# Kernel optimization log

Hardware: AMD Instinct MI355X
Metric: run time of the kernel (lower is better)

## Reference

```python
import jax, jax.numpy as jnp
import numpy as np

NUM_CLASSES = 4
LAMBDA_CREDA = 1.0
LAMBDA_ENTROPY = 0.1
SIGMA = 32.0          # config.sigma (fixed, not 'auto')
USE_UNCERTAINTY = True
EPS = 1e-8
LOG2 = float(np.log(2.0))

N_S, N_T, D = 4096, 4096, 1024


def _rbf(x, y, sigma):
    # squared euclidean distances (== torch.cdist(x,y)**2), then gaussian kernel
    d2 = (jnp.sum(x * x, axis=1)[:, None] + jnp.sum(y * y, axis=1)[None, :]
          - 2.0 * (x @ y.T))
    d2 = jnp.maximum(d2, 0.0)
    return jnp.exp(-d2 / (2.0 * sigma * sigma + EPS))


def _h2(tr, sumsq):
    # H2(A) = -log2(tr(A@A)), A = K/(tr(K)+eps); tr(A@A) = sum(K*K)/(tr+eps)^2 for symmetric K
    info = sumsq / (tr + EPS) ** 2
    return -jnp.log(info + EPS) / LOG2


def setup_inputs() -> dict:
    key = jax.random.key(0)
    k1, k2, k3, k4, k5 = jax.random.split(key, 5)
    return {
        "features_s": jax.random.normal(k1, (N_S, D), dtype=jnp.float32),
        "logits_s": jax.random.normal(k2, (N_S, NUM_CLASSES), dtype=jnp.float32),
        "features_t": jax.random.normal(k3, (N_T, D), dtype=jnp.float32),
        "logits_t": jax.random.normal(k4, (N_T, NUM_CLASSES), dtype=jnp.float32),
        "labels_s": jax.random.randint(k5, (N_S,), 0, NUM_CLASSES, dtype=jnp.int32),
    }


def reference(features_s, logits_s, features_t, logits_t, labels_s):
    # ---- classification loss (cross entropy on source) ----
    logp_s = jax.nn.log_softmax(logits_s, axis=1)
    loss_cls = -jnp.mean(jnp.take_along_axis(logp_s, labels_s[:, None], axis=1))

    # ---- target entropy loss ----
    probs_t = jax.nn.softmax(logits_t, axis=1)
    loss_ent = -jnp.mean(jnp.sum(probs_t * jnp.log(probs_t + EPS), axis=1))

    # ---- pseudo labels + uncertainty weights ----
    pseudo_t = jnp.argmax(jax.lax.stop_gradient(probs_t), axis=1)
    if USE_UNCERTAINTY:
        h2_probs = -jnp.log(jnp.sum(probs_t ** 2, axis=1) + EPS) / LOG2
        h2_max = np.log(float(NUM_CLASSES)) / LOG2
        w = 1.0 - h2_probs / (h2_max + EPS)          # [N_t]
    else:
        w = jnp.ones((features_t.shape[0],), dtype=probs_t.dtype)

    # ---- shared RBF kernel blocks (sigma fixed -> identical across classes) ----
    K_ss = _rbf(features_s, features_s, SIGMA)       # [N_s, N_s]
    K_tt = _rbf(features_t, features_t, SIGMA)       # [N_t, N_t]
    K_st = _rbf(features_s, features_t, SIGMA)       # [N_s, N_t]

    # per-class masks (zero-masking a kernel preserves trace and trace(K@K))
    Ms = jax.nn.one_hot(labels_s, NUM_CLASSES, dtype=K_ss.dtype).T   # [C, N_s]
    Mt = jax.nn.one_hot(pseudo_t, NUM_CLASSES, dtype=K_tt.dtype).T   # [C, N_t]
    Wt = Mt * w[None, :]                                             # [C, N_t]
    Wt2 = Wt * Wt

    n_s = jnp.sum(Ms, axis=1)                        # class counts (source)
    n_t = jnp.sum(Mt, axis=1)                        # class counts (target)

    # traces: diag(K)=1, target block weighted by outer(w,w)
    tr_s = n_s                                       # [C]
    tr_t = jnp.sum(Wt2, axis=1)                      # [C]

    # sum of squared entries of the masked (and weighted) blocks
    ss_s = jnp.einsum('ci,ci->c', Ms @ (K_ss ** 2), Ms)     # tr(K_s^2) per class
    ss_t = jnp.einsum('ci,ci->c', Wt2 @ (K_tt ** 2), Wt2)   # tr(K_tw^2) per class
    ss_st = jnp.einsum('ci,ci->c', Ms @ (K_st ** 2), Mt)    # sum(K_st^2) per class

    h_s = _h2(tr_s, ss_s)
    h_t = _h2(tr_t, ss_t)
    h_mix = _h2(tr_s + tr_t, ss_s + 2.0 * ss_st + ss_t)

    per_class = h_mix - 0.5 * (h_s + h_t)            # [C]
    valid = (n_s >= 2) & (n_t >= 2)
    n_valid = jnp.sum(valid.astype(per_class.dtype))
    creda_sum = jnp.sum(jnp.where(valid, per_class, 0.0))
    loss_creda = jnp.where(n_valid > 0, creda_sum / jnp.maximum(n_valid, 1.0), 0.0)

    total_loss = loss_cls + LAMBDA_CREDA * loss_creda + LAMBDA_ENTROPY * loss_ent
    return total_loss
```

## Files before the change

kernel.cpp:

```cpp
#include <hip/hip_runtime.h>
#include <cstdint>
#include <cstddef>

#define NS_ROWS 4096
#define NT_ROWS 4096
#define DIM 1024
#define NC 4
#define NWORK_MAX 2432
#define ACC_N 26

typedef __attribute__((ext_vector_type(4))) float f32x4;
typedef long long i64;

#define GLOBAL_AS __attribute__((address_space(1)))
#define LDS_AS __attribute__((address_space(3)))


__device__ __forceinline__ int argmax4(float4 l) {
    int am = 0; float bm = l.x;
    if (l.y > bm) { bm = l.y; am = 1; }
    if (l.z > bm) { bm = l.z; am = 2; }
    if (l.w > bm) { bm = l.w; am = 3; }
    return am;
}

__global__ void prep_rows(const float* __restrict__ LS, const int* __restrict__ labels,
                          const float* __restrict__ LT, float* __restrict__ acc) {
    __shared__ float sacc[ACC_N];
    int t = threadIdx.x;
    if (t < ACC_N) sacc[t] = 0.f;
    __syncthreads();
    int gid = blockIdx.x * 256 + t;
    const float EPSF = 1e-8f;
    if (gid < NS_ROWS) {
        float4 l = ((const float4*)LS)[gid];
        float m = fmaxf(fmaxf(l.x, l.y), fmaxf(l.z, l.w));
        float e = expf(l.x - m) + expf(l.y - m) + expf(l.z - m) + expf(l.w - m);
        float lse = m + logf(e);
        int lab = labels[gid];
        float ll = (lab == 0) ? l.x : (lab == 1) ? l.y : (lab == 2) ? l.z : l.w;
        atomicAdd(&sacc[0], lse - ll);
    } else {
        int j = gid - NS_ROWS;
        float4 l = ((const float4*)LT)[j];
        float m = fmaxf(fmaxf(l.x, l.y), fmaxf(l.z, l.w));
        float p0 = expf(l.x - m), p1 = expf(l.y - m), p2 = expf(l.z - m), p3 = expf(l.w - m);
        float s = p0 + p1 + p2 + p3;
        p0 /= s; p1 /= s; p2 /= s; p3 /= s;
        float ent = p0 * logf(p0 + EPSF) + p1 * logf(p1 + EPSF) +
                    p2 * logf(p2 + EPSF) + p3 * logf(p3 + EPSF);
        int am = argmax4(l);
        float sumsq = p0 * p0 + p1 * p1 + p2 * p2 + p3 * p3;
        const float INV_LOG2 = 1.44269504088896340736f;
        float h2 = -logf(sumsq + EPSF) * INV_LOG2;
        float w = 1.0f - h2 / (2.0f + EPSF);
        atomicAdd(&sacc[1], ent);
        atomicAdd(&sacc[10 + am], w * w);
    }
    __syncthreads();
    if (t < ACC_N && sacc[t] != 0.f) atomicAdd(&acc[t], sacc[t]);
}

__global__ void rank_rows(const int* __restrict__ labels, const float* __restrict__ LT,
                          int* __restrict__ ctrl, float* __restrict__ acc,
                          int* __restrict__ dstS, int* __restrict__ dstT) {
    __shared__ unsigned long long sdata[1024];
    int t = threadIdx.x;
    bool isS = (blockIdx.x == 0);
    int* dst = isS ? dstS : dstT;

    int c4[4];
    if (isS) {
        int4 lab4 = ((const int4*)labels)[t];
        c4[0] = lab4.x; c4[1] = lab4.y; c4[2] = lab4.z; c4[3] = lab4.w;
        if (t < ACC_N) acc[t] = 0.f;
    } else {
#pragma unroll
        for (int i = 0; i < 4; ++i)
            c4[i] = argmax4(((const float4*)LT)[t * 4 + i]);
    }
    unsigned long long packed = 0ULL;
#pragma unroll
    for (int i = 0; i < 4; ++i) packed += 1ULL << (c4[i] * 16);
    sdata[t] = packed;
    __syncthreads();
    for (int off = 1; off < 1024; off <<= 1) {
        unsigned long long v = sdata[t];
        unsigned long long add = (t >= off) ? sdata[t - off] : 0ULL;
        __syncthreads();
        sdata[t] = v + add;
        __syncthreads();
    }
    unsigned long long tot = sdata[1023];
    unsigned long long ex = (t > 0) ? sdata[t - 1] : 0ULL;
    int baseC[NC]; int b = 0;
#pragma unroll
    for (int c = 0; c < NC; ++c) {
        baseC[c] = b;
        b += (int)((tot >> (c * 16)) & 0xFFFFULL);
    }
    if (t == 0) {
#pragma unroll
        for (int c = 0; c < NC; ++c) {
            ctrl[(isS ? 0 : 4) + c] = (int)((tot >> (c * 16)) & 0xFFFFULL);
            ctrl[(isS ? 16 : 20) + c] = baseC[c];
        }
    }
    int pref[NC];
#pragma unroll
    for (int c = 0; c < NC; ++c)
        pref[c] = (int)((ex >> (c * 16)) & 0xFFFFULL) + baseC[c];
#pragma unroll
    for (int i = 0; i < 4; ++i) {
        int c = c4[i];
        dst[t * 4 + i] = pref[c]++;
    }
}

__global__ void aux_build(const int* __restrict__ ctrl, int4* __restrict__ wl,
                          int* __restrict__ ctrl_w) {
    int t = threadIdx.x;
    int Ts[NC], Tt[NC];
#pragma unroll
    for (int c = 0; c < NC; ++c) {
        Ts[c] = (ctrl[c] + 127) >> 7;
        Tt[c] = (ctrl[4 + c] + 127) >> 7;
    }
    int segSize[12];
#pragma unroll
    for (int c = 0; c < NC; ++c) {
        segSize[c * 3 + 0] = Ts[c] * (Ts[c] + 1) / 2;
        segSize[c * 3 + 1] = Tt[c] * (Tt[c] + 1) / 2;
        segSize[c * 3 + 2] = Ts[c] * Tt[c];
    }
    if (t == 0) {
        int n = 0;
        for (int s = 0; s < 12; ++s) n += segSize[s];
        ctrl_w[24] = n;
    }
    if (t >= 12) return;
    int base = 0;
    for (int s = 0; s < t; ++s) base += segSize[s];
    int c = t / 3, kind = t % 3;
    int4* w = wl + base;
    int n = 0;
    if (kind == 0) {
        for (int tj = 0; tj < Ts[c]; ++tj)
            for (int ti = 0; ti <= tj; ++ti) w[n++] = make_int4(0, c, ti, tj);
    } else if (kind == 1) {
        for (int tj = 0; tj < Tt[c]; ++tj)
            for (int ti = 0; ti <= tj; ++ti) w[n++] = make_int4(1, c, ti, tj);
    } else {
        for (int ti = 0; ti < Ts[c]; ++ti)
            for (int tj = 0; tj < Tt[c]; ++tj) w[n++] = make_int4(2, c, ti, tj);
    }
}

__global__ void scatter_feat(const float* __restrict__ FS, const float* __restrict__ FT,
                             const int* __restrict__ labels, const float* __restrict__ LT,
                             const int* __restrict__ dstS, const int* __restrict__ dstT,
                             unsigned char* __restrict__ fs, unsigned char* __restrict__ ft,
                             float* __restrict__ nS, float* __restrict__ wS, int* __restrict__ cS,
                             float* __restrict__ nT, float* __restrict__ wT, int* __restrict__ cT) {
    int row = blockIdx.x * 4 + (threadIdx.x >> 6);
    int lane = threadIdx.x & 63;
    bool isS = row < NS_ROWS;
    int r = isS ? row : row - NS_ROWS;
    int dst = isS ? dstS[r] : dstT[r];

    const float* src = (isS ? FS : FT) + (size_t)r * DIM;
    float4 v0 = ((const float4*)src)[lane * 4 + 0];
    float4 v1 = ((const float4*)src)[lane * 4 + 1];
    float4 v2 = ((const float4*)src)[lane * 4 + 2];
    float4 v3 = ((const float4*)src)[lane * 4 + 3];
    int w0 = 0, w1 = 0, w2 = 0, w3 = 0;
    w0 = __builtin_amdgcn_cvt_pk_fp8_f32(v0.x, v0.y, w0, false);
    w0 = __builtin_amdgcn_cvt_pk_fp8_f32(v0.z, v0.w, w0, true);
    w1 = __builtin_amdgcn_cvt_pk_fp8_f32(v1.x, v1.y, w1, false);
    w1 = __builtin_amdgcn_cvt_pk_fp8_f32(v1.z, v1.w, w1, true);
    w2 = __builtin_amdgcn_cvt_pk_fp8_f32(v2.x, v2.y, w2, false);
    w2 = __builtin_amdgcn_cvt_pk_fp8_f32(v2.z, v2.w, w2, true);
    w3 = __builtin_amdgcn_cvt_pk_fp8_f32(v3.x, v3.y, w3, false);
    w3 = __builtin_amdgcn_cvt_pk_fp8_f32(v3.z, v3.w, w3, true);

    float ssum = 0.f;
#define ACCQ(wv)                                                       \
    do {                                                               \
        float q0 = __builtin_amdgcn_cvt_f32_fp8((wv), 0);              \
        float q1 = __builtin_amdgcn_cvt_f32_fp8((wv), 1);              \
        float q2 = __builtin_amdgcn_cvt_f32_fp8((wv), 2);              \
        float q3 = __builtin_amdgcn_cvt_f32_fp8((wv), 3);              \
        ssum += q0 * q0 + q1 * q1 + q2 * q2 + q3 * q3;                 \
    } while (0)
    ACCQ(w0); ACCQ(w1); ACCQ(w2); ACCQ(w3);
#undef ACCQ

    unsigned char* fdst = (isS ? fs : ft) + (size_t)dst * DIM;
    *(uint4*)(fdst + lane * 16) = make_uint4((unsigned)w0, (unsigned)w1,
                                             (unsigned)w2, (unsigned)w3);

    for (int off = 32; off; off >>= 1) ssum += __shfl_xor(ssum, off);

    if (lane == 0) {
        if (isS) {
            nS[dst] = ssum; wS[dst] = 1.0f; cS[dst] = labels[r];
        } else {
            float4 l = ((const float4*)LT)[r];
            int am = argmax4(l);
            float m = fmaxf(fmaxf(l.x, l.y), fmaxf(l.z, l.w));
            float p0 = expf(l.x - m), p1 = expf(l.y - m),
                  p2 = expf(l.z - m), p3 = expf(l.w - m);
            float s = p0 + p1 + p2 + p3;
            float sumsq = (p0 * p0 + p1 * p1 + p2 * p2 + p3 * p3) / (s * s);
            const float INV_LOG2 = 1.44269504088896340736f;
            float h2 = -logf(sumsq + 1e-8f) * INV_LOG2;
            float w = 1.0f - h2 / (2.0f + 1e-8f);
            nT[dst] = ssum; wT[dst] = w * w; cT[dst] = am;
        }
    }
}

__global__ __launch_bounds__(256, 4)
void gemm_reduce(const unsigned char* __restrict__ fs, const unsigned char* __restrict__ ft,
                 const float* __restrict__ nS, const float* __restrict__ wS, const int* __restrict__ cS,
                 const float* __restrict__ nT, const float* __restrict__ wT, const int* __restrict__ cT,
                 const int* __restrict__ ctrl, const int4* __restrict__ wl,
                 float* __restrict__ acc) {
    __shared__ unsigned char As[2][128 * 32];
    __shared__ unsigned char Bs[2][128 * 32];
    __shared__ float sred;

    int nwork = ctrl[24];
    int chunk = (nwork + 7) >> 3;
    int sub = blockIdx.x >> 3, xcd = blockIdx.x & 7;
    if (sub >= chunk) return;
    int widx = xcd * chunk + sub;
    if (widx >= nwork) return;
    int4 it = wl[widx];
    int kind = it.x, cls = it.y, ti = it.z, tj = it.w;

    const unsigned char *A, *B;
    const float *nA, *nB, *wA, *wB;
    const int *cA, *cB;
    int baseA, baseB;
    if (kind == 0)      { A = fs; B = fs; nA = nS; nB = nS; wA = wS; wB = wS; cA = cS; cB = cS;
                          baseA = ctrl[16 + cls]; baseB = baseA; }
    else if (kind == 1) { A = ft; B = ft; nA = nT; nB = nT; wA = wT; wB = wT; cA = cT; cB = cT;
                          baseA = ctrl[20 + cls]; baseB = baseA; }
    else                { A = fs; B = ft; nA = nS; nB = nT; wA = wS; cA = cS; cB = cT;
                          wB = wS;
                          baseA = ctrl[16 + cls]; baseB = ctrl[20 + cls]; }
    float* outp = acc + 14 + kind * 4 + cls;
    float factor = (kind != 2 && ti != tj) ? 2.0f : 1.0f;

    int tid = threadIdx.x;
    int lane = tid & 63;
    int wid = tid >> 6;
    int wr = wid >> 1, wc = wid & 1;

    int rowA0 = baseA + ti * 128;
    int rowB0 = baseB + tj * 128;

    int srow = tid >> 1;
    int sb = (tid & 1) * 16;

    const unsigned char* pa = A + (size_t)min(rowA0 + srow, 4095) * DIM + sb;
    const unsigned char* pb = B + (size_t)min(rowB0 + srow, 4095) * DIM + sb;

    f32x4 accf[4][4];
#pragma unroll
    for (int m = 0; m < 4; ++m)
#pragma unroll
        for (int n = 0; n < 4; ++n) accf[m][n] = (f32x4)(0.f);

    int lr = lane & 15;
    int lk = (lane >> 4) * 8;

#define STAGE(buf, kt)                                                            \
    do {                                                                          \
        int k0_ = (kt) * 32;                                                      \
        __builtin_amdgcn_global_load_lds((const GLOBAL_AS void*)(pa + k0_),       \
            (LDS_AS void*)(As[buf] + tid * 16), 16, 0, 0);                        \
        __builtin_amdgcn_global_load_lds((const GLOBAL_AS void*)(pb + k0_),       \
            (LDS_AS void*)(Bs[buf] + tid * 16), 16, 0, 0);                        \
    } while (0)

#define COMPUTE(buf)                                                              \
    do {                                                                          \
        i64 af[4], bfr[4];                                                        \
        _Pragma("unroll")                                                         \
        for (int f = 0; f < 4; ++f)                                               \
            af[f] = *(const i64*)(As[buf] + (wr * 64 + f * 16 + lr) * 32 + lk);   \
        _Pragma("unroll")                                                         \
        for (int f = 0; f < 4; ++f)                                               \
            bfr[f] = *(const i64*)(Bs[buf] + (wc * 64 + f * 16 + lr) * 32 + lk);  \
        _Pragma("unroll")                                                         \
        for (int m = 0; m < 4; ++m)                                               \
            _Pragma("unroll")                                                     \
            for (int n = 0; n < 4; ++n)                                           \
                accf[m][n] = __builtin_amdgcn_mfma_f32_16x16x32_fp8_fp8(          \
                    af[m], bfr[n], accf[m][n], 0, 0, 0);                          \
    } while (0)

    STAGE(0, 0);
    asm volatile("s_waitcnt vmcnt(0)");
    __syncthreads();

    int cur = 0;
    for (int kt = 0; kt < DIM / 32 - 1; ++kt) {
        STAGE(cur ^ 1, kt + 1);
        COMPUTE(cur);
        __syncthreads();
        cur ^= 1;
    }
    COMPUTE(cur);

    int rowBase = rowA0 + wr * 64;
    int colBase = rowB0 + wc * 64;

    float cn[4], cw[4];
#pragma unroll
    for (int f = 0; f < 4; ++f) {
        int gj = colBase + f * 16 + lr;
        int gjc = min(gj, 4095);
        cn[f] = nB[gjc];
        cw[f] = (gj < 4096 && cB[gjc] == cls) ? wB[gjc] : 0.0f;
    }

    const float NEGF = (-2.0f / (2.0f * 32.0f * 32.0f + 1e-8f)) * 1.44269504088896340736f;
    float lacc = 0.f;

#pragma unroll
    for (int m = 0; m < 4; ++m) {
#pragma unroll
        for (int j = 0; j < 4; ++j) {
            int gi = rowBase + m * 16 + (lane >> 4) * 4 + j;
            int gic = min(gi, 4095);
            float rn = nA[gic];
            float rw = (gi < 4096 && cA[gic] == cls) ? wA[gic] : 0.0f;
#pragma unroll
            for (int n = 0; n < 4; ++n) {
                float dot = accf[m][n][j];
                float d2 = rn + cn[n] - 2.0f * dot;
                d2 = fmaxf(d2, 0.0f);
                float k2 = exp2f(d2 * NEGF);
                lacc += k2 * rw * cw[n];
            }
        }
    }

    if (tid == 0) sred = 0.f;
    __syncthreads();
    for (int off = 32; off; off >>= 1) lacc += __shfl_xor(lacc, off);
    if (lane == 0) atomicAdd(&sred, lacc);
    __syncthreads();
    if (tid == 0) atomicAdd(outp, factor * sred);
#undef STAGE
#undef COMPUTE
}

__global__ void finalize_kernel(const float* __restrict__ acc, const int* __restrict__ ctrl,
                                float* __restrict__ out) {
    if (threadIdx.x != 0 || blockIdx.x != 0) return;
    const double EPS = 1e-8;
    const double LOG2 = 0.6931471805599453;
    double loss_cls = (double)acc[0] / NS_ROWS;
    double loss_ent = -(double)acc[1] / NT_ROWS;
    double creda_sum = 0.0, n_valid = 0.0;
    for (int c = 0; c < NC; ++c) {
        int nsc_i = ctrl[c], ntc_i = ctrl[4 + c];
        double nsc = (double)nsc_i, trt = acc[10 + c];
        double sss = acc[14 + c], sst = acc[18 + c], ssst = acc[22 + c];
        double trs = nsc;
        double info_s = sss / ((trs + EPS) * (trs + EPS));
        double h_s = -log(info_s + EPS) / LOG2;
        double info_t = sst / ((trt + EPS) * (trt + EPS));
        double h_t = -log(info_t + EPS) / LOG2;
        double trm = trs + trt;
        double ssm = sss + 2.0 * ssst + sst;
        double info_m = ssm / ((trm + EPS) * (trm + EPS));
        double h_m = -log(info_m + EPS) / LOG2;
        double pc = h_m - 0.5 * (h_s + h_t);
        if (nsc_i >= 2 && ntc_i >= 2) { creda_sum += pc; n_valid += 1.0; }
    }
    double creda = (n_valid > 0.0) ? creda_sum / n_valid : 0.0;
    out[0] = (float)(loss_cls + 1.0 * creda + 0.1 * loss_ent);
}

extern "C" void kernel_launch(void* const* d_in, const int* in_sizes, int n_in,
                              void* d_out, int out_size, void* d_ws, size_t ws_size,
                              hipStream_t stream) {
    const float* FS = (const float*)d_in[0];
    const float* LS = (const float*)d_in[1];
    const float* FT = (const float*)d_in[2];
    const float* LT = (const float*)d_in[3];
    const int* LAB = (const int*)d_in[4];

    char* ws = (char*)d_ws;
    unsigned char* fs = (unsigned char*)(ws);
    unsigned char* ft = (unsigned char*)(ws + 4194304);
    char* p = ws + 8388608;
    float* nS  = (float*)(p);
    float* wS  = (float*)(p + 16384);
    int*   cS  = (int*)  (p + 32768);
    float* nT  = (float*)(p + 49152);
    float* wT  = (float*)(p + 65536);
    int*   cT  = (int*)  (p + 81920);
    int*   ctrl = (int*)  (p + 98304);
    float* acc  = (float*)(p + 98304 + 128);
    int4*  wl   = (int4*) (p + 98304 + 512);
    int*   dstS = (int*)  (p + 98304 + 512 + NWORK_MAX * 16);
    int*   dstT = dstS + NS_ROWS;

    rank_rows<<<2, 1024, 0, stream>>>(LAB, LT, ctrl, acc, dstS, dstT);
    aux_build<<<1, 64, 0, stream>>>(ctrl, wl, ctrl);
    prep_rows<<<32, 256, 0, stream>>>(LS, LAB, LT, acc);
    scatter_feat<<<2048, 256, 0, stream>>>(FS, FT, LAB, LT, dstS, dstT, fs, ft,
                                           nS, wS, cS, nT, wT, cT);
    gemm_reduce<<<NWORK_MAX, 256, 0, stream>>>(fs, ft, nS, wS, cS, nT, wT, cT,
                                               ctrl, wl, acc);
    finalize_kernel<<<1, 1, 0, stream>>>(acc, ctrl, (float*)d_out);
}
```

Before: 70.24 us.

## Fuse row prep into rank kernel, use wave-shuffle scan, deepen GEMM K tile

Merges the separate prep_rows kernel into the ranking kernel, which removes one launch and its global atomics. The LDS Hillis-Steele scan with many barriers is replaced by a wave-level shuffle scan plus a small cross-wave scan. Zeroing of the accumulator slots moves into aux_build. The fp8 GEMM stages 64-wide K tiles instead of 32, halving the number of barriers and loop iterations, at the cost of twice the LDS per block, which may reduce occupancy.

```diff
diff --git a/kernel.cpp b/kernel.cpp
--- a/kernel.cpp
+++ b/kernel.cpp
@@ -24,75 +24,84 @@
     return am;
 }
 
-__global__ void prep_rows(const float* __restrict__ LS, const int* __restrict__ labels,
-                          const float* __restrict__ LT, float* __restrict__ acc) {
-    __shared__ float sacc[ACC_N];
+__global__ __launch_bounds__(1024)
+void rank_prep(const int* __restrict__ labels, const float* __restrict__ LS,
+               const float* __restrict__ LT,
+               int* __restrict__ ctrl, float* __restrict__ acc,
+               int* __restrict__ dstS, int* __restrict__ dstT) {
+    __shared__ unsigned long long wtot[16];
+    __shared__ float wred[16];
+    __shared__ float cls4[NC];
     int t = threadIdx.x;
-    if (t < ACC_N) sacc[t] = 0.f;
-    __syncthreads();
-    int gid = blockIdx.x * 256 + t;
-    const float EPSF = 1e-8f;
-    if (gid < NS_ROWS) {
-        float4 l = ((const float4*)LS)[gid];
-        float m = fmaxf(fmaxf(l.x, l.y), fmaxf(l.z, l.w));
-        float e = expf(l.x - m) + expf(l.y - m) + expf(l.z - m) + expf(l.w - m);
-        float lse = m + logf(e);
-        int lab = labels[gid];
-        float ll = (lab == 0) ? l.x : (lab == 1) ? l.y : (lab == 2) ? l.z : l.w;
-        atomicAdd(&sacc[0], lse - ll);
-    } else {
-        int j = gid - NS_ROWS;
-        float4 l = ((const float4*)LT)[j];
-        float m = fmaxf(fmaxf(l.x, l.y), fmaxf(l.z, l.w));
-        float p0 = expf(l.x - m), p1 = expf(l.y - m), p2 = expf(l.z - m), p3 = expf(l.w - m);
-        float s = p0 + p1 + p2 + p3;
-        p0 /= s; p1 /= s; p2 /= s; p3 /= s;
-        float ent = p0 * logf(p0 + EPSF) + p1 * logf(p1 + EPSF) +
-                    p2 * logf(p2 + EPSF) + p3 * logf(p3 + EPSF);
-        int am = argmax4(l);
-        float sumsq = p0 * p0 + p1 * p1 + p2 * p2 + p3 * p3;
-        const float INV_LOG2 = 1.44269504088896340736f;
-        float h2 = -logf(sumsq + EPSF) * INV_LOG2;
-        float w = 1.0f - h2 / (2.0f + EPSF);
-        atomicAdd(&sacc[1], ent);
-        atomicAdd(&sacc[10 + am], w * w);
-    }
-    __syncthreads();
-    if (t < ACC_N && sacc[t] != 0.f) atomicAdd(&acc[t], sacc[t]);
-}
-
-__global__ void rank_rows(const int* __restrict__ labels, const float* __restrict__ LT,
-                          int* __restrict__ ctrl, float* __restrict__ acc,
-                          int* __restrict__ dstS, int* __restrict__ dstT) {
-    __shared__ unsigned long long sdata[1024];
-    int t = threadIdx.x;
+    int wid = t >> 6, lane = t & 63;
     bool isS = (blockIdx.x == 0);
     int* dst = isS ? dstS : dstT;
+    const float EPSF = 1e-8f;
+    const float INV_LOG2 = 1.44269504088896340736f;
+
+    if (t < NC) cls4[t] = 0.f;
 
     int c4[4];
+    float localScalar = 0.f;
+    float localW2[NC] = {0.f, 0.f, 0.f, 0.f};
     if (isS) {
         int4 lab4 = ((const int4*)labels)[t];
         c4[0] = lab4.x; c4[1] = lab4.y; c4[2] = lab4.z; c4[3] = lab4.w;
-        if (t < ACC_N) acc[t] = 0.f;
+#pragma unroll
+        for (int i = 0; i < 4; ++i) {
+            float4 l = ((const float4*)LS)[t * 4 + i];
+            float m = fmaxf(fmaxf(l.x, l.y), fmaxf(l.z, l.w));
+            float e = expf(l.x - m) + expf(l.y - m) + expf(l.z - m) + expf(l.w - m);
+            float lse = m + logf(e);
+            int lab = c4[i];
+            float ll = (lab == 0) ? l.x : (lab == 1) ? l.y : (lab == 2) ? l.z : l.w;
+            localScalar += lse - ll;
+        }
     } else {
 #pragma unroll
-        for (int i = 0; i < 4; ++i)
-            c4[i] = argmax4(((const float4*)LT)[t * 4 + i]);
-    }
+        for (int i = 0; i < 4; ++i) {
+            float4 l = ((const float4*)LT)[t * 4 + i];
+            int am = argmax4(l);
+            c4[i] = am;
+            float m = fmaxf(fmaxf(l.x, l.y), fmaxf(l.z, l.w));
+            float p0 = expf(l.x - m), p1 = expf(l.y - m),
+                  p2 = expf(l.z - m), p3 = expf(l.w - m);
+            float s = p0 + p1 + p2 + p3;
+            p0 /= s; p1 /= s; p2 /= s; p3 /= s;
+            localScalar += p0 * logf(p0 + EPSF) + p1 * logf(p1 + EPSF) +
+                           p2 * logf(p2 + EPSF) + p3 * logf(p3 + EPSF);
+            float sumsq = p0 * p0 + p1 * p1 + p2 * p2 + p3 * p3;
+            float h2 = -logf(sumsq + EPSF) * INV_LOG2;
+            float w = 1.0f - h2 / (2.0f + EPSF);
+            localW2[am] += w * w;
+        }
+    }
+
     unsigned long long packed = 0ULL;
 #pragma unroll
     for (int i = 0; i < 4; ++i) packed += 1ULL << (c4[i] * 16);
-    sdata[t] = packed;
-    __syncthreads();
-    for (int off = 1; off < 1024; off <<= 1) {
-        unsigned long long v = sdata[t];
-        unsigned long long add = (t >= off) ? sdata[t - off] : 0ULL;
-        __syncthreads();
-        sdata[t] = v + add;
-        __syncthreads();
-    }
-    unsigned long long tot = sdata[1023];
-    unsigned long long ex = (t > 0) ? sdata[t - 1] : 0ULL;
+    unsigned long long v = packed;
+#pragma unroll
+    for (int off = 1; off < 64; off <<= 1) {
+        unsigned long long n = __shfl_up(v, off);
+        if (lane >= off) v += n;
+    }
+    if (lane == 63) wtot[wid] = v;
+    __syncthreads();
+    if (t < 16) {
+        unsigned long long x = wtot[t];
+#pragma unroll
+        for (int off = 1; off < 16; off <<= 1) {
+            unsigned long long n = __shfl_up(x, off);
+            if (lane >= off) x += n;
+        }
+        wtot[t] = x;
+    }
+    __syncthreads();
+    unsigned long long incl = v + (wid > 0 ? wtot[wid - 1] : 0ULL);
+    unsigned long long tot = wtot[15];
+    unsigned long long ex = incl - packed;
+
     int baseC[NC]; int b = 0;
 #pragma unroll
     for (int c = 0; c < NC; ++c) {
@@ -115,11 +124,30 @@
         int c = c4[i];
         dst[t * 4 + i] = pref[c]++;
     }
+
+    for (int off = 32; off; off >>= 1) localScalar += __shfl_xor(localScalar, off);
+    if (lane == 0) wred[wid] = localScalar;
+    if (!isS) {
+#pragma unroll
+        for (int c = 0; c < NC; ++c) {
+            float x = localW2[c];
+            for (int off = 32; off; off >>= 1) x += __shfl_xor(x, off);
+            if (lane == 0 && x != 0.f) atomicAdd(&cls4[c], x);
+        }
+    }
+    __syncthreads();
+    if (t == 0) {
+        float s = 0.f;
+        for (int i = 0; i < 16; ++i) s += wred[i];
+        acc[isS ? 0 : 1] = s;
+    }
+    if (!isS && t < NC) acc[10 + t] = cls4[t];
 }
 
 __global__ void aux_build(const int* __restrict__ ctrl, int4* __restrict__ wl,
-                          int* __restrict__ ctrl_w) {
+                          int* __restrict__ ctrl_w, float* __restrict__ acc) {
     int t = threadIdx.x;
+    if (t >= 12 && t < 24) acc[14 + (t - 12)] = 0.f;
     int Ts[NC], Tt[NC];
 #pragma unroll
     for (int c = 0; c < NC; ++c) {
@@ -226,8 +254,8 @@
                  const float* __restrict__ nT, const float* __restrict__ wT, const int* __restrict__ cT,
                  const int* __restrict__ ctrl, const int4* __restrict__ wl,
                  float* __restrict__ acc) {
-    __shared__ unsigned char As[2][128 * 32];
-    __shared__ unsigned char Bs[2][128 * 32];
+    __shared__ unsigned char As[2][128 * 64];
+    __shared__ unsigned char Bs[2][128 * 64];
     __shared__ float sred;
 
     int nwork = ctrl[24];
@@ -261,11 +289,13 @@
     int rowA0 = baseA + ti * 128;
     int rowB0 = baseB + tj * 128;
 
-    int srow = tid >> 1;
-    int sb = (tid & 1) * 16;
-
-    const unsigned char* pa = A + (size_t)min(rowA0 + srow, 4095) * DIM + sb;
-    const unsigned char* pb = B + (size_t)min(rowB0 + srow, 4095) * DIM + sb;
+    int srow = tid >> 2;
+    int sb = (tid & 3) * 16;
+
+    const unsigned char* pa0 = A + (size_t)min(rowA0 + srow,      4095) * DIM + sb;
+    const unsigned char* pa1 = A + (size_t)min(rowA0 + srow + 64, 4095) * DIM + sb;
+    const unsigned char* pb0 = B + (size_t)min(rowB0 + srow,      4095) * DIM + sb;
+    const unsigned char* pb1 = B + (size_t)min(rowB0 + srow + 64, 4095) * DIM + sb;
 
     f32x4 accf[4][4];
 #pragma unroll
@@ -278,22 +308,26 @@
 
 #define STAGE(buf, kt)                                                            \
     do {                                                                          \
-        int k0_ = (kt) * 32;                                                      \
-        __builtin_amdgcn_global_load_lds((const GLOBAL_AS void*)(pa + k0_),       \
+        int k0_ = (kt) * 64;                                                      \
+        __builtin_amdgcn_global_load_lds((const GLOBAL_AS void*)(pa0 + k0_),      \
             (LDS_AS void*)(As[buf] + tid * 16), 16, 0, 0);                        \
-        __builtin_amdgcn_global_load_lds((const GLOBAL_AS void*)(pb + k0_),       \
+        __builtin_amdgcn_global_load_lds((const GLOBAL_AS void*)(pa1 + k0_),      \
+            (LDS_AS void*)(As[buf] + 4096 + tid * 16), 16, 0, 0);                 \
+        __builtin_amdgcn_global_load_lds((const GLOBAL_AS void*)(pb0 + k0_),      \
             (LDS_AS void*)(Bs[buf] + tid * 16), 16, 0, 0);                        \
+        __builtin_amdgcn_global_load_lds((const GLOBAL_AS void*)(pb1 + k0_),      \
+            (LDS_AS void*)(Bs[buf] + 4096 + tid * 16), 16, 0, 0);                 \
     } while (0)
 
-#define COMPUTE(buf)                                                              \
+#define COMPUTE_HALF(buf, kk)                                                     \
     do {                                                                          \
         i64 af[4], bfr[4];                                                        \
         _Pragma("unroll")                                                         \
         for (int f = 0; f < 4; ++f)                                               \
-            af[f] = *(const i64*)(As[buf] + (wr * 64 + f * 16 + lr) * 32 + lk);   \
+            af[f] = *(const i64*)(As[buf] + (wr * 64 + f * 16 + lr) * 64 + (kk) + lk); \
         _Pragma("unroll")                                                         \
         for (int f = 0; f < 4; ++f)                                               \
-            bfr[f] = *(const i64*)(Bs[buf] + (wc * 64 + f * 16 + lr) * 32 + lk);  \
+            bfr[f] = *(const i64*)(Bs[buf] + (wc * 64 + f * 16 + lr) * 64 + (kk) + lk); \
         _Pragma("unroll")                                                         \
         for (int m = 0; m < 4; ++m)                                               \
             _Pragma("unroll")                                                     \
@@ -307,13 +341,15 @@
     __syncthreads();
 
     int cur = 0;
-    for (int kt = 0; kt < DIM / 32 - 1; ++kt) {
+    for (int kt = 0; kt < DIM / 64 - 1; ++kt) {
         STAGE(cur ^ 1, kt + 1);
-        COMPUTE(cur);
+        COMPUTE_HALF(cur, 0);
+        COMPUTE_HALF(cur, 32);
         __syncthreads();
         cur ^= 1;
     }
-    COMPUTE(cur);
+    COMPUTE_HALF(cur, 0);
+    COMPUTE_HALF(cur, 32);
 
     int rowBase = rowA0 + wr * 64;
     int colBase = rowB0 + wc * 64;
@@ -356,7 +392,7 @@
     __syncthreads();
     if (tid == 0) atomicAdd(outp, factor * sred);
 #undef STAGE
-#undef COMPUTE
+#undef COMPUTE_HALF
 }
 
 __global__ void finalize_kernel(const float* __restrict__ acc, const int* __restrict__ ctrl,
@@ -412,9 +448,8 @@
     int*   dstS = (int*)  (p + 98304 + 512 + NWORK_MAX * 16);
     int*   dstT = dstS + NS_ROWS;
 
-    rank_rows<<<2, 1024, 0, stream>>>(LAB, LT, ctrl, acc, dstS, dstT);
-    aux_build<<<1, 64, 0, stream>>>(ctrl, wl, ctrl);
-    prep_rows<<<32, 256, 0, stream>>>(LS, LAB, LT, acc);
+    rank_prep<<<2, 1024, 0, stream>>>(LAB, LS, LT, ctrl, acc, dstS, dstT);
+    aux_build<<<1, 64, 0, stream>>>(ctrl, wl, ctrl, acc);
     scatter_feat<<<2048, 256, 0, stream>>>(FS, FT, LAB, LT, dstS, dstT, fs, ft,
                                            nS, wS, cS, nT, wT, cT);
     gemm_reduce<<<NWORK_MAX, 256, 0, stream>>>(fs, ft, nS, wS, cS, nT, wT, cT,
```

Measured after the change: 95.17 us. 35.5% more time.
